# Kernel optimization log

Measured on AMD Instinct MI355X. Metric: run time of the kernel, lower is better.

## Reference

```python
import jax, jax.numpy as jnp
import numpy as np

POOL = 8  # kernel_size = [8, 1]: pool factor 8 along H (for *_H) and along W (for *_W)

def _pool_h(x, k):
    B, C, H, W = x.shape
    return x.reshape(B, C, H // k, k, W).mean(axis=3)  # (B,C,H/k,W)

def _pool_w(x, k):
    B, C, H, W = x.shape
    return x.reshape(B, C, H, W // k, k).mean(axis=4)  # (B,C,H,W/k)

def setup_inputs() -> dict:
    key = jax.random.key(0)
    k1, k2 = jax.random.split(key)
    shape = (8, 256, 128, 128)
    return {
        "tensor1": jax.random.normal(k1, shape, dtype=jnp.float32),
        "tensor2": jax.random.normal(k2, shape, dtype=jnp.float32),
    }

def reference(tensor1, tensor2):
    B, C, H, W = tensor1.shape
    kH, kW = H // POOL, W // POOL
    # pooled keys (from tensor1) and values (from tensor2)
    key_H = _pool_h(tensor1, POOL)    # (B,C,kH,W)
    key_W = _pool_w(tensor1, POOL)    # (B,C,H,kW)
    val_H = _pool_h(tensor2, POOL)    # (B,C,kH,W)
    val_W = _pool_w(tensor2, POOL)    # (B,C,H,kW)
    # criss-cross energies: contract over (c, w) for H-branch, (c, h) for W-branch
    energy_H = jnp.einsum('bchw,bckw->bhk', tensor2, key_H).reshape(B, H * kH)
    energy_W = jnp.einsum('bchw,bchk->bwk', tensor2, key_W).reshape(B, W * kW)
    energy = jnp.concatenate([energy_H, energy_W], axis=-1)
    # global (all-element) min-max normalization, then softmax over concat axis
    e_min, e_max = energy.min(), energy.max()
    energy = (energy - e_min) / (e_max - e_min)
    concate = jax.nn.softmax(energy, axis=-1)
    att_H = concate[:, : H * kH].reshape(B, H, kH)
    att_W = concate[:, H * kH :].reshape(B, W, kW)
    out_H = jnp.einsum('bckw,bhk->bchw', val_H, att_H)
    out_W = jnp.einsum('bchk,bwk->bchw', val_W, att_W)
    gamma = jnp.float32(0.5)
    return gamma * (out_H + out_W) + tensor2
```

## Files before the change

kernel.cpp:

```cpp
#include <hip/hip_runtime.h>
#include <cstddef>

#define CC 256
#define HH 128
#define WW 128
#define HW (HH*WW)

typedef __attribute__((ext_vector_type(8))) short short8v;
typedef __attribute__((ext_vector_type(4))) float float4v;

__device__ __forceinline__ short f2bf(float x) {
    unsigned u = __float_as_uint(x);
    u += 0x7FFFu + ((u >> 16) & 1u);
    return (short)(u >> 16);
}
__device__ __forceinline__ float4 add4(float4 a, float4 b) {
    float4 r; r.x=a.x+b.x; r.y=a.y+b.y; r.z=a.z+b.z; r.w=a.w+b.w; return r;
}
__device__ __forceinline__ float4 scale4(float4 a, float s) {
    float4 r; r.x=a.x*s; r.y=a.y*s; r.z=a.z*s; r.w=a.w*s; return r;
}
__device__ __forceinline__ float4 shflx4(float4 v, int m) {
    float4 r;
    r.x = __shfl_xor(v.x, m); r.y = __shfl_xor(v.y, m);
    r.z = __shfl_xor(v.z, m); r.w = __shfl_xor(v.w, m);
    return r;
}
__device__ __forceinline__ float hsum4(float4 v) { return v.x+v.y+v.z+v.w; }

__global__ __launch_bounds__(512) void fused_pool_energy(
    const float* __restrict__ t1, const float* __restrict__ t2,
    unsigned short* __restrict__ valHT, unsigned short* __restrict__ valWbf,
    float* __restrict__ PH, float* __restrict__ PW)
{
    __shared__ __align__(16) short t2lds[64*128];
    __shared__ __align__(16) short t2T  [128*64];
    __shared__ __align__(16) short kH   [16*128];
    __shared__ __align__(16) short kWT  [16*128];

    const int bid   = blockIdx.x;
    const int b     = bid & 7;
    const int chunk = bid >> 3;
    const int c0    = chunk * 2;
    const int tid   = threadIdx.x;
    const int l     = tid & 63;
    const int v     = tid >> 6;
    const int w4    = l & 31;
    const int rq    = l >> 5;

    float4v accH = {0.f,0.f,0.f,0.f};
    float4v accW = {0.f,0.f,0.f,0.f};

    for (int ci = 0; ci < 2; ++ci) {
        const int c = c0 + ci;
        const int bc = b*CC + c;
        const size_t cbase = (size_t)bc * HW;

        #pragma unroll
        for (int half = 0; half < 2; ++half) {
            const int hbase = half*64 + v*8 + rq*4;
            const float4* src = (const float4*)(t1 + cbase + (size_t)hbase * WW) + w4;
            float4 x0 = src[0], x1 = src[32], x2 = src[64], x3 = src[96];
            float4 s4 = add4(add4(x0,x1), add4(x2,x3));
            float4 m4 = scale4(add4(s4, shflx4(s4,32)), 0.125f);
            if (rq == 0) {
                const int k = half*8 + v;
                short4 p; p.x=f2bf(m4.x); p.y=f2bf(m4.y); p.z=f2bf(m4.z); p.w=f2bf(m4.w);
                *(short4*)&kH[k*128 + ((w4*4) ^ ((k&7)<<3))] = p;
            }
            float rs0 = hsum4(x0), rs1 = hsum4(x1), rs2 = hsum4(x2), rs3 = hsum4(x3);
            float o0 = __shfl_xor(rs0,1), o1 = __shfl_xor(rs1,1);
            float o2 = __shfl_xor(rs2,1), o3 = __shfl_xor(rs3,1);
            if ((l & 1) == 0) {
                const int kw = w4 >> 1;
                const int sw = (kw & 7) << 3;
                kWT[kw*128 + ((hbase+0) ^ sw)] = f2bf((rs0+o0)*0.125f);
                kWT[kw*128 + ((hbase+1) ^ sw)] = f2bf((rs1+o1)*0.125f);
                kWT[kw*128 + ((hbase+2) ^ sw)] = f2bf((rs2+o2)*0.125f);
                kWT[kw*128 + ((hbase+3) ^ sw)] = f2bf((rs3+o3)*0.125f);
            }
        }
        __syncthreads();

        #pragma unroll
        for (int half = 0; half < 2; ++half) {
            const int hbase = half*64 + v*8 + rq*4;
            const int hl4   = v*8 + rq*4;
            const float4* src = (const float4*)(t2 + cbase + (size_t)hbase * WW) + w4;
            float4 x0 = src[0], x1 = src[32], x2 = src[64], x3 = src[96];

            float4 s4 = add4(add4(x0,x1), add4(x2,x3));
            float4 m4 = scale4(add4(s4, shflx4(s4,32)), 0.125f);
            if (rq == 0) {
                const int k = half*8 + v;
                const size_t vb = (size_t)bc * 2048;
                valHT[vb + (w4*4+0)*16 + k] = (unsigned short)f2bf(m4.x);
                valHT[vb + (w4*4+1)*16 + k] = (unsigned short)f2bf(m4.y);
                valHT[vb + (w4*4+2)*16 + k] = (unsigned short)f2bf(m4.z);
                valHT[vb + (w4*4+3)*16 + k] = (unsigned short)f2bf(m4.w);
            }
            {
                float rs0 = hsum4(x0), rs1 = hsum4(x1), rs2 = hsum4(x2), rs3 = hsum4(x3);
                float o0 = __shfl_xor(rs0,1), o1 = __shfl_xor(rs1,1);
                float o2 = __shfl_xor(rs2,1), o3 = __shfl_xor(rs3,1);
                if ((l & 1) == 0) {
                    const int kw = w4 >> 1;
                    const size_t vb = (size_t)bc*2048 + (size_t)hbase*16 + kw;
                    valWbf[vb +  0] = (unsigned short)f2bf((rs0+o0)*0.125f);
                    valWbf[vb + 16] = (unsigned short)f2bf((rs1+o1)*0.125f);
                    valWbf[vb + 32] = (unsigned short)f2bf((rs2+o2)*0.125f);
                    valWbf[vb + 48] = (unsigned short)f2bf((rs3+o3)*0.125f);
                }
            }
            short s0x=f2bf(x0.x), s0y=f2bf(x0.y), s0z=f2bf(x0.z), s0w=f2bf(x0.w);
            short s1x=f2bf(x1.x), s1y=f2bf(x1.y), s1z=f2bf(x1.z), s1w=f2bf(x1.w);
            short s2x=f2bf(x2.x), s2y=f2bf(x2.y), s2z=f2bf(x2.z), s2w=f2bf(x2.w);
            short s3x=f2bf(x3.x), s3y=f2bf(x3.y), s3z=f2bf(x3.z), s3w=f2bf(x3.w);
            {
                short4 p;
                p.x=s0x; p.y=s0y; p.z=s0z; p.w=s0w;
                *(short4*)&t2lds[(hl4+0)*128 + ((w4*4) ^ (((hl4+0)&7)<<3))] = p;
                p.x=s1x; p.y=s1y; p.z=s1z; p.w=s1w;
                *(short4*)&t2lds[(hl4+1)*128 + ((w4*4) ^ (((hl4+1)&7)<<3))] = p;
                p.x=s2x; p.y=s2y; p.z=s2z; p.w=s2w;
                *(short4*)&t2lds[(hl4+2)*128 + ((w4*4) ^ (((hl4+2)&7)<<3))] = p;
                p.x=s3x; p.y=s3y; p.z=s3z; p.w=s3w;
                *(short4*)&t2lds[(hl4+3)*128 + ((w4*4) ^ (((hl4+3)&7)<<3))] = p;
            }
            {
                short4 p;
                int w = w4*4 + 0;
                p.x=s0x; p.y=s1x; p.z=s2x; p.w=s3x;
                *(short4*)&t2T[w*64 + (hl4 ^ (((w>>1)&7)<<3))] = p;
                w = w4*4 + 1;
                p.x=s0y; p.y=s1y; p.z=s2y; p.w=s3y;
                *(short4*)&t2T[w*64 + (hl4 ^ (((w>>1)&7)<<3))] = p;
                w = w4*4 + 2;
                p.x=s0z; p.y=s1z; p.z=s2z; p.w=s3z;
                *(short4*)&t2T[w*64 + (hl4 ^ (((w>>1)&7)<<3))] = p;
                w = w4*4 + 3;
                p.x=s0w; p.y=s1w; p.z=s2w; p.w=s3w;
                *(short4*)&t2T[w*64 + (hl4 ^ (((w>>1)&7)<<3))] = p;
            }
            __syncthreads();

            if ((v >> 2) == half) {
                const int hl = (v & 3)*16 + (l & 15);
                const int kb = l & 15;
                #pragma unroll
                for (int ws2 = 0; ws2 < 4; ++ws2) {
                    const int wb = ws2*32 + (l>>4)*8;
                    short8v A  = *(const short8v*)&t2lds[hl*128 + (wb ^ ((hl&7)<<3))];
                    short8v B  = *(const short8v*)&kH  [kb*128 + (wb ^ ((kb&7)<<3))];
                    accH = __builtin_amdgcn_mfma_f32_16x16x32_bf16(A, B, accH, 0, 0, 0);
                }
            }
            {
                const int kb = l & 15;
                const int w  = v*16 + (l & 15);
                #pragma unroll
                for (int hs = 0; hs < 2; ++hs) {
                    const int hloc = hs*32 + (l>>4)*8;
                    const int hg   = half*64 + hloc;
                    short8v A = *(const short8v*)&kWT[kb*128 + (hg  ^ ((kb&7)<<3))];
                    short8v B = *(const short8v*)&t2T[w*64   + (hloc ^ (((w>>1)&7)<<3))];
                    accW = __builtin_amdgcn_mfma_f32_16x16x32_bf16(A, B, accW, 0, 0, 0);
                }
            }
            __syncthreads();
        }
    }

    {
        const size_t pb = ((size_t)(b*128 + chunk)) * 2048;
        #pragma unroll
        for (int r = 0; r < 4; ++r) {
            const int h = v*16 + (l>>4)*4 + r;
            PH[pb + h*16 + (l&15)] = accH[r];
            const int k = (l>>4)*4 + r;
            PW[pb + k*128 + v*16 + (l&15)] = accW[r];
        }
    }
}

__global__ __launch_bounds__(256) void energy_reduce(
    const float* __restrict__ PH, const float* __restrict__ PW,
    float* __restrict__ energy, float* __restrict__ bmin, float* __restrict__ bmax)
{
    const int bidx = blockIdx.x;
    const int tid  = threadIdx.x;
    const int ol   = tid & 63, qd = tid >> 6;
    const int o    = bidx*64 + ol;
    __shared__ float red[4][64];

    const int isW = o >> 14;
    const int oo  = o & 16383;
    const int b   = oo >> 11, i = oo & 2047;
    const float* P = (isW ? PW : PH) + (size_t)b*128*2048 + i;
    float s = 0.f;
    #pragma unroll
    for (int j = 0; j < 32; ++j) s += P[(size_t)(qd*32 + j)*2048];
    red[qd][ol] = s;
    __syncthreads();

    if (tid < 64) {
        float v = red[0][tid] + red[1][tid] + red[2][tid] + red[3][tid];
        const int o2 = bidx*64 + tid;
        const int oo2 = o2 & 16383;
        const int b2 = oo2 >> 11, i2 = oo2 & 2047;
        const size_t dst = (o2 >> 14)
            ? ((size_t)b2*4096 + 2048 + (size_t)(i2 & 127)*16 + (i2 >> 7))
            : ((size_t)b2*4096 + i2);
        energy[dst] = v;
        float mn = v, mx = v;
        #pragma unroll
        for (int sft = 32; sft > 0; sft >>= 1) {
            mn = fminf(mn, __shfl_xor(mn, sft));
            mx = fmaxf(mx, __shfl_xor(mx, sft));
        }
        if (tid == 0) { bmin[bidx] = mn; bmax[bidx] = mx; }
    }
}

__global__ __launch_bounds__(1024) void softmax_kernel(
    const float* __restrict__ energy, const float* __restrict__ bmin,
    const float* __restrict__ bmax,
    unsigned short* __restrict__ aHbf, unsigned short* __restrict__ aWbf)
{
    const int b = blockIdx.x, tid = threadIdx.x;
    const int lane = tid & 63, wid = tid >> 6;
    __shared__ float smn[16], smx[16], sred[16], bc2[2];

    float mn = 3.0e38f, mx = -3.0e38f;
    if (tid < 512) { mn = bmin[tid]; mx = bmax[tid]; }
    #pragma unroll
    for (int s = 32; s > 0; s >>= 1) {
        mn = fminf(mn, __shfl_xor(mn, s));
        mx = fmaxf(mx, __shfl_xor(mx, s));
    }
    if (lane == 0) { smn[wid] = mn; smx[wid] = mx; }
    __syncthreads();
    if (tid == 0) {
        float a = smn[0], m = smx[0];
        #pragma unroll
        for (int i = 1; i < 16; ++i) { a = fminf(a, smn[i]); m = fmaxf(m, smx[i]); }
        bc2[0] = a; bc2[1] = m;
    }
    __syncthreads();
    const float gmn = bc2[0];
    const float inv = 1.0f / (bc2[1] - gmn);

    float4 v = ((const float4*)energy)[b*1024 + tid];
    float4 e;
    e.x = __expf((v.x - gmn) * inv);
    e.y = __expf((v.y - gmn) * inv);
    e.z = __expf((v.z - gmn) * inv);
    e.w = __expf((v.w - gmn) * inv);
    float loc = e.x + e.y + e.z + e.w;
    #pragma unroll
    for (int s = 32; s > 0; s >>= 1) loc += __shfl_down(loc, s);
    if (lane == 0) sred[wid] = loc;
    __syncthreads();
    if (tid == 0) {
        float a = 0.f;
        #pragma unroll
        for (int j = 0; j < 16; ++j) a += sred[j];
        bc2[0] = 1.0f / a;
    }
    __syncthreads();
    const float r = bc2[0];
    short4 p;
    p.x = f2bf(e.x * r); p.y = f2bf(e.y * r);
    p.z = f2bf(e.z * r); p.w = f2bf(e.w * r);
    if (tid < 512)
        *(short4*)&aHbf[(size_t)b*2048 + tid*4] = p;
    else
        *(short4*)&aWbf[(size_t)b*2048 + (tid-512)*4] = p;
}

__global__ __launch_bounds__(256) void out_kernel(
    const float* __restrict__ t2,
    const unsigned short* __restrict__ valHT,
    const unsigned short* __restrict__ valWbf,
    const unsigned short* __restrict__ aHbf,
    const unsigned short* __restrict__ aWbf,
    float* __restrict__ out)
{
    const int bid = blockIdx.x;
    const int b = bid & 7, c = bid >> 3;
    const int bc = b*CC + c;
    const int tid = threadIdx.x;
    const int l  = tid & 63;
    const int wv = tid >> 6;
    const int ln = l & 15;
    const int q4 = l >> 4;
    const size_t tb = (size_t)bc * HW;

    const unsigned short* vHT = valHT  + (size_t)bc*2048;
    const unsigned short* vW  = valWbf + (size_t)bc*2048;
    const unsigned short* aH  = aHbf + (size_t)b*2048;
    const unsigned short* aW  = aWbf + (size_t)b*2048;

    short8v Bf[8];
    {
        const unsigned short* src = (q4 < 2) ? vHT : aW;
        #pragma unroll
        for (int tw = 0; tw < 8; ++tw)
            Bf[tw] = *(const short8v*)&src[(tw*16 + ln)*16 + (q4 & 1)*8];
    }

    #pragma unroll
    for (int t = 0; t < 2; ++t) {
        const int th = wv*2 + t;
        const unsigned short* asrc = (q4 < 2) ? aH : vW;
        short8v Af = *(const short8v*)&asrc[(th*16 + ln)*16 + (q4 & 1)*8];
        #pragma unroll
        for (int tw = 0; tw < 8; ++tw) {
            float4v acc = {0.f,0.f,0.f,0.f};
            acc = __builtin_amdgcn_mfma_f32_16x16x32_bf16(Af, Bf[tw], acc, 0, 0, 0);
            const size_t base = tb + (size_t)(th*16 + q4*4)*128 + tw*16 + ln;
            #pragma unroll
            for (int r = 0; r < 4; ++r) {
                const float tv = t2[base + (size_t)r*128];
                out[base + (size_t)r*128] = fmaf(0.5f, acc[r], tv);
            }
        }
    }
}

extern "C" void kernel_launch(void* const* d_in, const int* in_sizes, int n_in,
                              void* d_out, int out_size, void* d_ws, size_t ws_size,
                              hipStream_t stream)
{
    const float* t1 = (const float*)d_in[0];
    const float* t2 = (const float*)d_in[1];
    float* out = (float*)d_out;
    char*  ws  = (char*)d_ws;

    unsigned short* valHT  = (unsigned short*)ws;
    unsigned short* valWbf = (unsigned short*)(ws + ((size_t)8 << 20));
    float* energy = (float*)(ws + ((size_t)16 << 20));
    float* bmin   = energy + 32768;
    float* bmax   = bmin + 512;
    unsigned short* aHbf = (unsigned short*)(ws + ((size_t)17 << 20));
    unsigned short* aWbf = aHbf + 8*2048;

    float* PH = out;
    float* PW = out + (size_t)2097152;

    hipLaunchKernelGGL(fused_pool_energy, dim3(1024), dim3(512), 0, stream,
                       t1, t2, valHT, valWbf, PH, PW);
    hipLaunchKernelGGL(energy_reduce, dim3(512), dim3(256), 0, stream,
                       PH, PW, energy, bmin, bmax);
    hipLaunchKernelGGL(softmax_kernel, dim3(8), dim3(1024), 0, stream,
                       energy, bmin, bmax, aHbf, aWbf);
    hipLaunchKernelGGL(out_kernel, dim3(2048), dim3(256), 0, stream,
                       t2, valHT, valWbf, aHbf, aWbf, out);
}
```

Baseline: 130.8 us.

## Write pooled values coalesced in fp32 and transpose to bf16 in separate kernel

The fused pooling/energy kernel no longer does scattered 2-byte strided stores of the pooled values. It writes val_H as coalesced float4 rows and stages val_W through a swizzled LDS buffer before writing it out contiguously. A new val_transpose kernel then converts both to bf16 in the transposed layout that the output kernel expects. This is meant to remove uncoalesced global store traffic, at the cost of an extra kernel launch, extra fp32 workspace traffic and a larger workspace footprint.

```diff
diff --git a/kernel.cpp b/kernel.cpp
--- a/kernel.cpp
+++ b/kernel.cpp
@@ -30,13 +30,14 @@
 
 __global__ __launch_bounds__(512) void fused_pool_energy(
     const float* __restrict__ t1, const float* __restrict__ t2,
-    unsigned short* __restrict__ valHT, unsigned short* __restrict__ valWbf,
+    float* __restrict__ valH, float* __restrict__ valWT,
     float* __restrict__ PH, float* __restrict__ PW)
 {
     __shared__ __align__(16) short t2lds[64*128];
     __shared__ __align__(16) short t2T  [128*64];
     __shared__ __align__(16) short kH   [16*128];
     __shared__ __align__(16) short kWT  [16*128];
+    __shared__ __align__(16) float vWs  [16*64];
 
     const int bid   = blockIdx.x;
     const int b     = bid & 7;
@@ -53,8 +54,7 @@
 
     for (int ci = 0; ci < 2; ++ci) {
         const int c = c0 + ci;
-        const int bc = b*CC + c;
-        const size_t cbase = (size_t)bc * HW;
+        const size_t cbase = ((size_t)b * CC + c) * HW;
 
         #pragma unroll
         for (int half = 0; half < 2; ++half) {
@@ -93,11 +93,7 @@
             float4 m4 = scale4(add4(s4, shflx4(s4,32)), 0.125f);
             if (rq == 0) {
                 const int k = half*8 + v;
-                const size_t vb = (size_t)bc * 2048;
-                valHT[vb + (w4*4+0)*16 + k] = (unsigned short)f2bf(m4.x);
-                valHT[vb + (w4*4+1)*16 + k] = (unsigned short)f2bf(m4.y);
-                valHT[vb + (w4*4+2)*16 + k] = (unsigned short)f2bf(m4.z);
-                valHT[vb + (w4*4+3)*16 + k] = (unsigned short)f2bf(m4.w);
+                *(float4*)&valH[((size_t)(b*CC + c)*16 + k)*128 + w4*4] = m4;
             }
             {
                 float rs0 = hsum4(x0), rs1 = hsum4(x1), rs2 = hsum4(x2), rs3 = hsum4(x3);
@@ -105,11 +101,11 @@
                 float o2 = __shfl_xor(rs2,1), o3 = __shfl_xor(rs3,1);
                 if ((l & 1) == 0) {
                     const int kw = w4 >> 1;
-                    const size_t vb = (size_t)bc*2048 + (size_t)hbase*16 + kw;
-                    valWbf[vb +  0] = (unsigned short)f2bf((rs0+o0)*0.125f);
-                    valWbf[vb + 16] = (unsigned short)f2bf((rs1+o1)*0.125f);
-                    valWbf[vb + 32] = (unsigned short)f2bf((rs2+o2)*0.125f);
-                    valWbf[vb + 48] = (unsigned short)f2bf((rs3+o3)*0.125f);
+                    const int sw = (kw & 7) << 3;
+                    vWs[kw*64 + ((hl4+0) ^ sw)] = (rs0+o0)*0.125f;
+                    vWs[kw*64 + ((hl4+1) ^ sw)] = (rs1+o1)*0.125f;
+                    vWs[kw*64 + ((hl4+2) ^ sw)] = (rs2+o2)*0.125f;
+                    vWs[kw*64 + ((hl4+3) ^ sw)] = (rs3+o3)*0.125f;
                 }
             }
             short s0x=f2bf(x0.x), s0y=f2bf(x0.y), s0z=f2bf(x0.z), s0w=f2bf(x0.w);
@@ -167,6 +163,13 @@
                     accW = __builtin_amdgcn_mfma_f32_16x16x32_bf16(A, B, accW, 0, 0, 0);
                 }
             }
+            {
+                const int k0 = tid >> 6,          h0 = tid & 63;
+                const int k1 = (tid+512) >> 6,    h1 = tid & 63;
+                const size_t gb = (size_t)(b*CC + c) * 16;
+                valWT[(gb + k0)*128 + half*64 + h0] = vWs[k0*64 + (h0 ^ ((k0&7)<<3))];
+                valWT[(gb + k1)*128 + half*64 + h1] = vWs[k1*64 + (h1 ^ ((k1&7)<<3))];
+            }
             __syncthreads();
         }
     }
@@ -180,6 +183,33 @@
             const int k = (l>>4)*4 + r;
             PW[pb + k*128 + v*16 + (l&15)] = accW[r];
         }
+    }
+}
+
+__global__ __launch_bounds__(256) void val_transpose(
+    const float* __restrict__ valH, const float* __restrict__ valWT,
+    unsigned short* __restrict__ valHT, unsigned short* __restrict__ valWbf)
+{
+    __shared__ float buf[2048];
+    const int bc  = blockIdx.x;
+    const int tid = threadIdx.x;
+    const float* srcs[2] = { valH + (size_t)bc*2048, valWT + (size_t)bc*2048 };
+    unsigned short* dsts[2] = { valHT + (size_t)bc*2048, valWbf + (size_t)bc*2048 };
+
+    #pragma unroll
+    for (int p = 0; p < 2; ++p) {
+        const float4* s4 = (const float4*)srcs[p];
+        *(float4*)&buf[tid*4]        = s4[tid];
+        *(float4*)&buf[1024 + tid*4] = s4[256 + tid];
+        __syncthreads();
+        const int w  = tid >> 1;
+        const int k0 = (tid & 1) * 8;
+        short8v o;
+        #pragma unroll
+        for (int j = 0; j < 8; ++j)
+            o[j] = f2bf(buf[(k0 + j)*128 + w]);
+        *(short8v*)&dsts[p][(size_t)w*16 + k0] = o;
+        __syncthreads();
     }
 }
 
@@ -337,19 +367,23 @@
     float* out = (float*)d_out;
     char*  ws  = (char*)d_ws;
 
-    unsigned short* valHT  = (unsigned short*)ws;
-    unsigned short* valWbf = (unsigned short*)(ws + ((size_t)8 << 20));
-    float* energy = (float*)(ws + ((size_t)16 << 20));
+    float* valH   = (float*)ws;
+    float* valWT  = (float*)(ws + ((size_t)16 << 20));
+    unsigned short* valHT  = (unsigned short*)(ws + ((size_t)32 << 20));
+    unsigned short* valWbf = (unsigned short*)(ws + ((size_t)40 << 20));
+    float* energy = (float*)(ws + ((size_t)48 << 20));
     float* bmin   = energy + 32768;
     float* bmax   = bmin + 512;
-    unsigned short* aHbf = (unsigned short*)(ws + ((size_t)17 << 20));
+    unsigned short* aHbf = (unsigned short*)(ws + ((size_t)49 << 20));
     unsigned short* aWbf = aHbf + 8*2048;
 
     float* PH = out;
     float* PW = out + (size_t)2097152;
 
     hipLaunchKernelGGL(fused_pool_energy, dim3(1024), dim3(512), 0, stream,
-                       t1, t2, valHT, valWbf, PH, PW);
+                       t1, t2, valH, valWT, PH, PW);
+    hipLaunchKernelGGL(val_transpose, dim3(2048), dim3(256), 0, stream,
+                       valH, valWT, valHT, valWbf);
     hipLaunchKernelGGL(energy_reduce, dim3(512), dim3(256), 0, stream,
                        PH, PW, energy, bmin, bmax);
     hipLaunchKernelGGL(softmax_kernel, dim3(8), dim3(1024), 0, stream,
```

Result: slower. 156.0 us (+19.3%).
